# Kernel optimization log

Measured on AMD Instinct MI355X. Metric: run time of the kernel, lower is better.

The kernel has to match this reference:

```python
import jax, jax.numpy as jnp
import numpy as np

B, O, D = 64, 36, 512
G1, G2 = 512, 512  # interactor sizes
F1, F2 = 512, 512  # aggregator sizes
BN_EPS = 1e-5


def setup_inputs() -> dict:
    key = jax.random.key(0)
    ks = jax.random.split(key, 10)
    sc = 0.02
    return {
        "objs": jax.random.normal(ks[0], (B, O, D), jnp.float32),
        "W1": jax.random.normal(ks[1], (G1, 2 * D), jnp.float32) * sc,
        "b1": jax.random.normal(ks[2], (G1,), jnp.float32) * sc,
        "W2": jax.random.normal(ks[3], (G2, G1), jnp.float32) * sc,
        "b2": jax.random.normal(ks[4], (G2,), jnp.float32) * sc,
        "gamma": jnp.ones((G2,), jnp.float32),
        "beta": jnp.zeros((G2,), jnp.float32),
        "W3": jax.random.normal(ks[5], (F1, G2), jnp.float32) * sc,
        "b3": jax.random.normal(ks[6], (F1,), jnp.float32) * sc,
        "W4": jax.random.normal(ks[7], (F2, F1), jnp.float32) * sc,
        "b4": jax.random.normal(ks[8], (F2,), jnp.float32) * sc,
    }


def reference(objs, W1, b1, W2, b2, gamma, beta, W3, b3, W4, b4):
    b, o, d = objs.shape
    # make_pairs: x_full[b,k,m] = concat(v[b,m], v[b,k]) -> (b, o*o, 2d)
    v_i = jnp.broadcast_to(objs[:, None, :, :], (b, o, o, d))  # varies over m
    v_j = jnp.broadcast_to(objs[:, :, None, :], (b, o, o, d))  # varies over k
    pairs = jnp.concatenate([v_i, v_j], axis=-1).reshape(b, o * o, 2 * d)
    # interaction MLP g
    h = jax.nn.relu(jnp.einsum('bpc,gc->bpg', pairs, W1) + b1)
    x_pairs = jax.nn.relu(jnp.einsum('bpg,hg->bph', h, W2) + b2)
    # sum over pairs, BatchNorm1d (training mode: batch stats, biased var)
    s = x_pairs.sum(axis=1)  # (b, G2)
    mean = s.mean(axis=0)
    var = ((s - mean) ** 2).mean(axis=0)
    sn = (s - mean) / jnp.sqrt(var + BN_EPS) * gamma + beta
    # aggregation MLP f
    a = jax.nn.relu(sn @ W3.T + b3)
    agg = jax.nn.relu(a @ W4.T + b4)
    return agg, x_pairs
```

## Files before the change

kernel.cpp:

```cpp
#include <hip/hip_runtime.h>
#include <cstdint>
#include <cstddef>

#define B_  64
#define O_  36
#define D_  512
#define P_  (O_*O_)
#define BO_ (B_*O_)

typedef short s8v __attribute__((ext_vector_type(8)));
typedef float f4v __attribute__((ext_vector_type(4)));

__device__ __forceinline__ void bsplit(float x, short& hi, short& lo) {
    unsigned u = __float_as_uint(x);
    unsigned r = (u + 0x7FFFu + ((u >> 16) & 1u)) >> 16;
    hi = (short)r;
    float hf = __uint_as_float(r << 16);
    float d = x - hf;
    unsigned u2 = __float_as_uint(d);
    unsigned r2 = (u2 + 0x7FFFu + ((u2 >> 16) & 1u)) >> 16;
    lo = (short)r2;
}

__global__ __launch_bounds__(256) void wsplit_all(
    const float* __restrict__ W2, const float* __restrict__ W1,
    short* __restrict__ W2h, short* __restrict__ W2l,
    short* __restrict__ W1h, short* __restrict__ W1l)
{
    int i = (blockIdx.x * 256 + threadIdx.x) * 4;
    float4 w;
    short* hip_; short* lop_; int o;
    if (i < 512 * 512) {
        w = *(const float4*)&W2[i];
        hip_ = W2h; lop_ = W2l; o = i;
    } else {
        o = i - 512 * 512;
        const int n = o >> 9, d = o & 511;
        w = *(const float4*)&W1[(size_t)(n & 511) * 1024 + ((n >> 9) << 9) + d];
        hip_ = W1h; lop_ = W1l;
    }
    short h0, l0, h1, l1, h2, l2, h3, l3;
    bsplit(w.x, h0, l0); bsplit(w.y, h1, l1);
    bsplit(w.z, h2, l2); bsplit(w.w, h3, l3);
    *(short4*)&hip_[o] = make_short4(h0, h1, h2, h3);
    *(short4*)&lop_[o] = make_short4(l0, l1, l2, l3);
}

__global__ __launch_bounds__(256, 2) void uv_mfma(
    const float* __restrict__ objs,
    const short* __restrict__ W1h, const short* __restrict__ W1l,
    float* __restrict__ U, float* __restrict__ V)
{
    __shared__ short Ah[128 * 40];
    __shared__ short Al[128 * 40];
    __shared__ short Bh[128 * 40];
    __shared__ short Bl[128 * 40];

    const int tid  = threadIdx.x;
    const int lane = tid & 63;
    const int wid  = tid >> 6;
    const int wr   = wid >> 1, wc = wid & 1;
    const int rowbase = blockIdx.y * 128;
    const int colbase = blockIdx.x * 128;

    const int srow = tid >> 1;
    const int skq  = (tid & 1) * 8;
    const float* Xrow  = objs + (size_t)(rowbase + srow) * 512;
    const short* Whrow = W1h + (size_t)(colbase + srow) * 512;
    const short* Wlrow = W1l + (size_t)(colbase + srow) * 512;

    const int fr = lane & 15;
    const int sl = (lane >> 4) * 8;
    const int abase = (wr * 64 + fr) * 40 + sl;
    const int bbase = (wc * 64 + fr) * 40 + sl;

    f4v acc[4][4];
    const f4v zero = {0.f, 0.f, 0.f, 0.f};
    #pragma unroll
    for (int i = 0; i < 4; ++i)
        #pragma unroll
        for (int j = 0; j < 4; ++j) acc[i][j] = zero;

    for (int kt = 0; kt < 512; kt += 32) {
        __syncthreads();
        #pragma unroll
        for (int pass = 0; pass < 2; ++pass) {
            const int kq = skq + pass * 16;
            const float4 x0 = *(const float4*)&Xrow[kt + kq];
            const float4 x1 = *(const float4*)&Xrow[kt + kq + 4];
            float hx[8] = {x0.x, x0.y, x0.z, x0.w, x1.x, x1.y, x1.z, x1.w};
            s8v hi8, lo8;
            #pragma unroll
            for (int j = 0; j < 8; ++j) { short h, l; bsplit(hx[j], h, l); hi8[j] = h; lo8[j] = l; }
            *(s8v*)&Ah[srow * 40 + kq] = hi8;
            *(s8v*)&Al[srow * 40 + kq] = lo8;
            *(s8v*)&Bh[srow * 40 + kq] = *(const s8v*)&Whrow[kt + kq];
            *(s8v*)&Bl[srow * 40 + kq] = *(const s8v*)&Wlrow[kt + kq];
        }
        __syncthreads();

        s8v ah[4], al[4], bh[4], bl[4];
        #pragma unroll
        for (int f = 0; f < 4; ++f) {
            ah[f] = *(const s8v*)&Ah[abase + f * 640];
            al[f] = *(const s8v*)&Al[abase + f * 640];
            bh[f] = *(const s8v*)&Bh[bbase + f * 640];
            bl[f] = *(const s8v*)&Bl[bbase + f * 640];
        }
        #pragma unroll
        for (int fm = 0; fm < 4; ++fm)
            #pragma unroll
            for (int fn = 0; fn < 4; ++fn)
                acc[fm][fn] = __builtin_amdgcn_mfma_f32_16x16x32_bf16(ah[fm], bh[fn], acc[fm][fn], 0, 0, 0);
        #pragma unroll
        for (int fm = 0; fm < 4; ++fm)
            #pragma unroll
            for (int fn = 0; fn < 4; ++fn)
                acc[fm][fn] = __builtin_amdgcn_mfma_f32_16x16x32_bf16(ah[fm], bl[fn], acc[fm][fn], 0, 0, 0);
        #pragma unroll
        for (int fm = 0; fm < 4; ++fm)
            #pragma unroll
            for (int fn = 0; fn < 4; ++fn)
                acc[fm][fn] = __builtin_amdgcn_mfma_f32_16x16x32_bf16(al[fm], bh[fn], acc[fm][fn], 0, 0, 0);
    }

    float* dst = (colbase < 512) ? U : V;
    const int cb = colbase & 511;
    const int r4 = (lane >> 4) * 4;
    #pragma unroll
    for (int fm = 0; fm < 4; ++fm) {
        #pragma unroll
        for (int r = 0; r < 4; ++r) {
            const int row = rowbase + wr * 64 + fm * 16 + r4 + r;
            float* drow = &dst[(size_t)row * 512 + cb + wc * 64 + fr];
            #pragma unroll
            for (int fn = 0; fn < 4; ++fn) drow[fn * 16] = acc[fm][fn][r];
        }
    }
}

__global__ __launch_bounds__(512, 2) void pair_gemm(
    const float* __restrict__ U, const float* __restrict__ V,
    const float* __restrict__ b1,
    const short* __restrict__ W2h, const short* __restrict__ W2l,
    const float* __restrict__ b2,
    float* __restrict__ xout, float* __restrict__ s)
{
    __shared__ short Ah[128 * 40];
    __shared__ short Al[128 * 40];
    __shared__ short Bh[512 * 40];
    __shared__ short Bl[512 * 40];
    __shared__ float b1s[512];

    const int tid  = threadIdx.x;
    const int lane = tid & 63;
    const int wid  = tid >> 6;
    const int wr   = wid >> 2;
    const int wc   = wid & 3;
    const int b     = blockIdx.y;
    const int pbase = blockIdx.x * 128;

    b1s[tid] = b1[tid];

    const int arow = tid & 127;
    const int akq  = (tid >> 7) << 3;
    const int p    = pbase + arow;
    const bool valid = (p < P_);
    int ki = 0, mi = 0;
    if (valid) { ki = p / O_; mi = p - ki * O_; }
    const float* Urow = U + (size_t)(b * O_ + mi) * 512 + akq;
    const float* Vrow = V + (size_t)(b * O_ + ki) * 512 + akq;

    const short* Whrow = W2h + (size_t)tid * 512;
    const short* Wlrow = W2l + (size_t)tid * 512;

    const int fr = lane & 15;
    const int sl = (lane >> 4) << 3;
    const int abase = (wr * 64 + fr) * 40 + sl;
    const int bbase = (wc * 128 + fr) * 40 + sl;

    f4v acc[4][8];
    const f4v zero = {0.f, 0.f, 0.f, 0.f};
    #pragma unroll
    for (int i = 0; i < 4; ++i)
        #pragma unroll
        for (int j = 0; j < 8; ++j) acc[i][j] = zero;

    for (int kt = 0; kt < 512; kt += 32) {
        __syncthreads();
        {
            s8v hi8, lo8;
            if (valid) {
                const float4 u0 = *(const float4*)&Urow[kt];
                const float4 u1 = *(const float4*)&Urow[kt + 4];
                const float4 v0 = *(const float4*)&Vrow[kt];
                const float4 v1 = *(const float4*)&Vrow[kt + 4];
                const float4 c0 = *(const float4*)&b1s[kt + akq];
                const float4 c1 = *(const float4*)&b1s[kt + akq + 4];
                float hx[8];
                hx[0] = fmaxf(u0.x + v0.x + c0.x, 0.f);
                hx[1] = fmaxf(u0.y + v0.y + c0.y, 0.f);
                hx[2] = fmaxf(u0.z + v0.z + c0.z, 0.f);
                hx[3] = fmaxf(u0.w + v0.w + c0.w, 0.f);
                hx[4] = fmaxf(u1.x + v1.x + c1.x, 0.f);
                hx[5] = fmaxf(u1.y + v1.y + c1.y, 0.f);
                hx[6] = fmaxf(u1.z + v1.z + c1.z, 0.f);
                hx[7] = fmaxf(u1.w + v1.w + c1.w, 0.f);
                #pragma unroll
                for (int j = 0; j < 8; ++j) { short h, l; bsplit(hx[j], h, l); hi8[j] = h; lo8[j] = l; }
            } else {
                #pragma unroll
                for (int j = 0; j < 8; ++j) { hi8[j] = 0; lo8[j] = 0; }
            }
            *(s8v*)&Ah[arow * 40 + akq] = hi8;
            *(s8v*)&Al[arow * 40 + akq] = lo8;
        }
        #pragma unroll
        for (int c = 0; c < 4; ++c) {
            *(s8v*)&Bh[tid * 40 + c * 8] = *(const s8v*)&Whrow[kt + c * 8];
            *(s8v*)&Bl[tid * 40 + c * 8] = *(const s8v*)&Wlrow[kt + c * 8];
        }
        __syncthreads();

        s8v ah[4], al[4];
        #pragma unroll
        for (int f = 0; f < 4; ++f) {
            ah[f] = *(const s8v*)&Ah[abase + f * 640];
            al[f] = *(const s8v*)&Al[abase + f * 640];
        }
        #pragma unroll
        for (int fn = 0; fn < 8; ++fn) {
            const s8v bh = *(const s8v*)&Bh[bbase + fn * 640];
            const s8v bl = *(const s8v*)&Bl[bbase + fn * 640];
            #pragma unroll
            for (int fm = 0; fm < 4; ++fm)
                acc[fm][fn] = __builtin_amdgcn_mfma_f32_16x16x32_bf16(ah[fm], bh, acc[fm][fn], 0, 0, 0);
            #pragma unroll
            for (int fm = 0; fm < 4; ++fm)
                acc[fm][fn] = __builtin_amdgcn_mfma_f32_16x16x32_bf16(ah[fm], bl, acc[fm][fn], 0, 0, 0);
            #pragma unroll
            for (int fm = 0; fm < 4; ++fm)
                acc[fm][fn] = __builtin_amdgcn_mfma_f32_16x16x32_bf16(al[fm], bh, acc[fm][fn], 0, 0, 0);
        }
    }

    float b2v[8];
    #pragma unroll
    for (int fn = 0; fn < 8; ++fn) b2v[fn] = b2[wc * 128 + fn * 16 + fr];
    const int r4 = (lane >> 4) << 2;
    float csum[8] = {0.f, 0.f, 0.f, 0.f, 0.f, 0.f, 0.f, 0.f};
    #pragma unroll
    for (int fm = 0; fm < 4; ++fm) {
        const int prow0 = pbase + wr * 64 + fm * 16 + r4;
        #pragma unroll
        for (int r = 0; r < 4; ++r) {
            const int pp = prow0 + r;
            if (pp < P_) {
                float* xrow = &xout[(size_t)(b * P_ + pp) * 512 + wc * 128 + fr];
                #pragma unroll
                for (int fn = 0; fn < 8; ++fn) {
                    float x = fmaxf(acc[fm][fn][r] + b2v[fn], 0.f);
                    xrow[fn * 16] = x;
                    csum[fn] += x;
                }
            }
        }
    }
    #pragma unroll
    for (int fn = 0; fn < 8; ++fn) {
        csum[fn] += __shfl_xor(csum[fn], 16);
        csum[fn] += __shfl_xor(csum[fn], 32);
    }
    if (lane < 16) {
        #pragma unroll
        for (int fn = 0; fn < 8; ++fn)
            atomicAdd(&s[b * 512 + wc * 128 + fn * 16 + lane], csum[fn]);
    }
}

__global__ __launch_bounds__(512) void bn_kernel(
    const float* __restrict__ s, const float* __restrict__ gamma,
    const float* __restrict__ beta, float* __restrict__ sn)
{
    const int g = threadIdx.x;
    float mean = 0.f;
    for (int b = 0; b < B_; ++b) mean += s[b * 512 + g];
    mean *= (1.f / B_);
    float var = 0.f;
    for (int b = 0; b < B_; ++b) { const float d = s[b * 512 + g] - mean; var = fmaf(d, d, var); }
    var *= (1.f / B_);
    const float inv = 1.f / sqrtf(var + 1e-5f);
    const float ga = gamma[g], be = beta[g];
    for (int b = 0; b < B_; ++b)
        sn[b * 512 + g] = (s[b * 512 + g] - mean) * inv * ga + be;
}

__global__ __launch_bounds__(256) void mlp512(
    const float* __restrict__ x, const float* __restrict__ W,
    const float* __restrict__ bias, float* __restrict__ out)
{
    __shared__ float xs[512];
    const int b = blockIdx.y;
    const int f = blockIdx.x * 256 + threadIdx.x;
    for (int g = threadIdx.x; g < 512; g += 256) xs[g] = x[b * 512 + g];
    __syncthreads();
    float sum = 0.f;
    #pragma unroll 8
    for (int k = 0; k < 512; k += 4) {
        const float4 w4 = *(const float4*)&W[(size_t)f * 512 + k];
        const float4 x4 = *(const float4*)&xs[k];
        sum = fmaf(w4.x, x4.x, sum); sum = fmaf(w4.y, x4.y, sum);
        sum = fmaf(w4.z, x4.z, sum); sum = fmaf(w4.w, x4.w, sum);
    }
    out[b * 512 + f] = fmaxf(sum + bias[f], 0.f);
}

extern "C" void kernel_launch(void* const* d_in, const int* in_sizes, int n_in,
                              void* d_out, int out_size, void* d_ws, size_t ws_size,
                              hipStream_t stream)
{
    const float* objs  = (const float*)d_in[0];
    const float* W1    = (const float*)d_in[1];
    const float* b1    = (const float*)d_in[2];
    const float* W2    = (const float*)d_in[3];
    const float* b2    = (const float*)d_in[4];
    const float* gamma = (const float*)d_in[5];
    const float* beta  = (const float*)d_in[6];
    const float* W3    = (const float*)d_in[7];
    const float* b3    = (const float*)d_in[8];
    const float* W4    = (const float*)d_in[9];
    const float* b4    = (const float*)d_in[10];

    float* out  = (float*)d_out;
    float* xout = out + B_ * 512;

    float* U  = (float*)d_ws;
    float* V  = U  + (size_t)BO_ * 512;
    float* s  = V  + (size_t)BO_ * 512;
    float* sn = s  + B_ * 512;
    float* a  = sn + B_ * 512;
    short* W2h = (short*)(a + B_ * 512);
    short* W2l = W2h + (size_t)512 * 512;
    short* W1h = W2l + (size_t)512 * 512;
    short* W1l = W1h + (size_t)1024 * 512;

    wsplit_all<<<768, 256, 0, stream>>>(W2, W1, W2h, W2l, W1h, W1l);
    uv_mfma<<<dim3(8, 18), 256, 0, stream>>>(objs, W1h, W1l, U, V);
    hipMemsetAsync(s, 0, B_ * 512 * sizeof(float), stream);
    pair_gemm<<<dim3(11, 64), 512, 0, stream>>>(U, V, b1, W2h, W2l, b2, xout, s);
    bn_kernel<<<1, 512, 0, stream>>>(s, gamma, beta, sn);
    mlp512<<<dim3(2, B_), 256, 0, stream>>>(sn, W3, b3, a);
    mlp512<<<dim3(2, B_), 256, 0, stream>>>(a, W4, b4, out);
}
```

Before: 469.4 us.

## Retile pair GEMM to 128x128 output tiles with octet-major LDS layout

The pair GEMM block now covers 128 pairs by 128 output columns with 256 threads, instead of 128 pairs by 512 columns with 512 threads. The grid grows fourfold, adding a column dimension, and LDS is reorganized into an octet-major [k-octet][row][8] layout to avoid bank conflicts without padding. The aim is better occupancy and load balance through smaller register and LDS footprints per block. In exchange, each block now recomputes the fused U+V+b1 ReLU and bf16 split of its A tile, so that work is repeated four times across the column blocks.

Result: faster. 451.3 us (-3.9%).

```diff
diff --git a/kernel.cpp b/kernel.cpp
--- a/kernel.cpp
+++ b/kernel.cpp
@@ -139,64 +139,73 @@
     }
 }
 
-__global__ __launch_bounds__(512, 2) void pair_gemm(
+__global__ __launch_bounds__(256, 3) void pair_gemm(
     const float* __restrict__ U, const float* __restrict__ V,
     const float* __restrict__ b1,
     const short* __restrict__ W2h, const short* __restrict__ W2l,
     const float* __restrict__ b2,
     float* __restrict__ xout, float* __restrict__ s)
 {
-    __shared__ short Ah[128 * 40];
-    __shared__ short Al[128 * 40];
-    __shared__ short Bh[512 * 40];
-    __shared__ short Bl[512 * 40];
+    __shared__ short Ah[4][128][8];
+    __shared__ short Al[4][128][8];
+    __shared__ short Bh[4][128][8];
+    __shared__ short Bl[4][128][8];
     __shared__ float b1s[512];
 
     const int tid  = threadIdx.x;
     const int lane = tid & 63;
     const int wid  = tid >> 6;
-    const int wr   = wid >> 2;
-    const int wc   = wid & 3;
-    const int b     = blockIdx.y;
-    const int pbase = blockIdx.x * 128;
-
-    b1s[tid] = b1[tid];
+    const int wr   = wid >> 1, wc = wid & 1;
+    const int b       = blockIdx.z;
+    const int pbase   = blockIdx.y * 128;
+    const int colbase = blockIdx.x * 128;
+
+    for (int g = tid; g < 512; g += 256) b1s[g] = b1[g];
 
     const int arow = tid & 127;
-    const int akq  = (tid >> 7) << 3;
+    const int a0   = (tid >> 7) * 2;
     const int p    = pbase + arow;
     const bool valid = (p < P_);
     int ki = 0, mi = 0;
     if (valid) { ki = p / O_; mi = p - ki * O_; }
-    const float* Urow = U + (size_t)(b * O_ + mi) * 512 + akq;
-    const float* Vrow = V + (size_t)(b * O_ + ki) * 512 + akq;
-
-    const short* Whrow = W2h + (size_t)tid * 512;
-    const short* Wlrow = W2l + (size_t)tid * 512;
+    const float* Urow = U + (size_t)(b * O_ + mi) * 512;
+    const float* Vrow = V + (size_t)(b * O_ + ki) * 512;
+
+    const int boct = wid;
+    const int brow = lane;
+    const short* Wh0 = W2h + (size_t)(colbase + brow) * 512 + boct * 8;
+    const short* Wh1 = Wh0 + (size_t)64 * 512;
+    const short* Wl0 = W2l + (size_t)(colbase + brow) * 512 + boct * 8;
+    const short* Wl1 = Wl0 + (size_t)64 * 512;
 
     const int fr = lane & 15;
-    const int sl = (lane >> 4) << 3;
-    const int abase = (wr * 64 + fr) * 40 + sl;
-    const int bbase = (wc * 128 + fr) * 40 + sl;
-
-    f4v acc[4][8];
+    const int q  = lane >> 4;
+
+    f4v acc[4][4];
     const f4v zero = {0.f, 0.f, 0.f, 0.f};
     #pragma unroll
     for (int i = 0; i < 4; ++i)
         #pragma unroll
-        for (int j = 0; j < 8; ++j) acc[i][j] = zero;
+        for (int j = 0; j < 4; ++j) acc[i][j] = zero;
 
     for (int kt = 0; kt < 512; kt += 32) {
         __syncthreads();
-        {
+        const s8v wh0 = *(const s8v*)&Wh0[kt];
+        const s8v wh1 = *(const s8v*)&Wh1[kt];
+        const s8v wl0 = *(const s8v*)&Wl0[kt];
+        const s8v wl1 = *(const s8v*)&Wl1[kt];
+        #pragma unroll
+        for (int j = 0; j < 2; ++j) {
+            const int oct = a0 + j;
+            const int k0  = kt + oct * 8;
             s8v hi8, lo8;
             if (valid) {
-                const float4 u0 = *(const float4*)&Urow[kt];
-                const float4 u1 = *(const float4*)&Urow[kt + 4];
-                const float4 v0 = *(const float4*)&Vrow[kt];
-                const float4 v1 = *(const float4*)&Vrow[kt + 4];
-                const float4 c0 = *(const float4*)&b1s[kt + akq];
-                const float4 c1 = *(const float4*)&b1s[kt + akq + 4];
+                const float4 u0 = *(const float4*)&Urow[k0];
+                const float4 u1 = *(const float4*)&Urow[k0 + 4];
+                const float4 v0 = *(const float4*)&Vrow[k0];
+                const float4 v1 = *(const float4*)&Vrow[k0 + 4];
+                const float4 c0 = *(const float4*)&b1s[k0];
+                const float4 c1 = *(const float4*)&b1s[k0 + 4];
                 float hx[8];
                 hx[0] = fmaxf(u0.x + v0.x + c0.x, 0.f);
                 hx[1] = fmaxf(u0.y + v0.y + c0.y, 0.f);
@@ -207,48 +216,50 @@
                 hx[6] = fmaxf(u1.z + v1.z + c1.z, 0.f);
                 hx[7] = fmaxf(u1.w + v1.w + c1.w, 0.f);
                 #pragma unroll
-                for (int j = 0; j < 8; ++j) { short h, l; bsplit(hx[j], h, l); hi8[j] = h; lo8[j] = l; }
+                for (int e = 0; e < 8; ++e) { short h, l; bsplit(hx[e], h, l); hi8[e] = h; lo8[e] = l; }
             } else {
                 #pragma unroll
-                for (int j = 0; j < 8; ++j) { hi8[j] = 0; lo8[j] = 0; }
+                for (int e = 0; e < 8; ++e) { hi8[e] = 0; lo8[e] = 0; }
             }
-            *(s8v*)&Ah[arow * 40 + akq] = hi8;
-            *(s8v*)&Al[arow * 40 + akq] = lo8;
-        }
-        #pragma unroll
-        for (int c = 0; c < 4; ++c) {
-            *(s8v*)&Bh[tid * 40 + c * 8] = *(const s8v*)&Whrow[kt + c * 8];
-            *(s8v*)&Bl[tid * 40 + c * 8] = *(const s8v*)&Wlrow[kt + c * 8];
-        }
+            *(s8v*)&Ah[oct][arow][0] = hi8;
+            *(s8v*)&Al[oct][arow][0] = lo8;
+        }
+        *(s8v*)&Bh[boct][brow][0]      = wh0;
+        *(s8v*)&Bh[boct][64 + brow][0] = wh1;
+        *(s8v*)&Bl[boct][brow][0]      = wl0;
+        *(s8v*)&Bl[boct][64 + brow][0] = wl1;
         __syncthreads();
 
-        s8v ah[4], al[4];
+        s8v ah[4], al[4], bh[4], bl[4];
         #pragma unroll
         for (int f = 0; f < 4; ++f) {
-            ah[f] = *(const s8v*)&Ah[abase + f * 640];
-            al[f] = *(const s8v*)&Al[abase + f * 640];
-        }
-        #pragma unroll
-        for (int fn = 0; fn < 8; ++fn) {
-            const s8v bh = *(const s8v*)&Bh[bbase + fn * 640];
-            const s8v bl = *(const s8v*)&Bl[bbase + fn * 640];
-            #pragma unroll
-            for (int fm = 0; fm < 4; ++fm)
-                acc[fm][fn] = __builtin_amdgcn_mfma_f32_16x16x32_bf16(ah[fm], bh, acc[fm][fn], 0, 0, 0);
-            #pragma unroll
-            for (int fm = 0; fm < 4; ++fm)
-                acc[fm][fn] = __builtin_amdgcn_mfma_f32_16x16x32_bf16(ah[fm], bl, acc[fm][fn], 0, 0, 0);
-            #pragma unroll
-            for (int fm = 0; fm < 4; ++fm)
-                acc[fm][fn] = __builtin_amdgcn_mfma_f32_16x16x32_bf16(al[fm], bh, acc[fm][fn], 0, 0, 0);
-        }
-    }
-
-    float b2v[8];
-    #pragma unroll
-    for (int fn = 0; fn < 8; ++fn) b2v[fn] = b2[wc * 128 + fn * 16 + fr];
-    const int r4 = (lane >> 4) << 2;
-    float csum[8] = {0.f, 0.f, 0.f, 0.f, 0.f, 0.f, 0.f, 0.f};
+            ah[f] = *(const s8v*)&Ah[q][wr * 64 + f * 16 + fr][0];
+            al[f] = *(const s8v*)&Al[q][wr * 64 + f * 16 + fr][0];
+            bh[f] = *(const s8v*)&Bh[q][wc * 64 + f * 16 + fr][0];
+            bl[f] = *(const s8v*)&Bl[q][wc * 64 + f * 16 + fr][0];
+        }
+        #pragma unroll
+        for (int fm = 0; fm < 4; ++fm)
+            #pragma unroll
+            for (int fn = 0; fn < 4; ++fn)
+                acc[fm][fn] = __builtin_amdgcn_mfma_f32_16x16x32_bf16(ah[fm], bh[fn], acc[fm][fn], 0, 0, 0);
+        #pragma unroll
+        for (int fm = 0; fm < 4; ++fm)
+            #pragma unroll
+            for (int fn = 0; fn < 4; ++fn)
+                acc[fm][fn] = __builtin_amdgcn_mfma_f32_16x16x32_bf16(ah[fm], bl[fn], acc[fm][fn], 0, 0, 0);
+        #pragma unroll
+        for (int fm = 0; fm < 4; ++fm)
+            #pragma unroll
+            for (int fn = 0; fn < 4; ++fn)
+                acc[fm][fn] = __builtin_amdgcn_mfma_f32_16x16x32_bf16(al[fm], bh[fn], acc[fm][fn], 0, 0, 0);
+    }
+
+    float b2v[4];
+    #pragma unroll
+    for (int fn = 0; fn < 4; ++fn) b2v[fn] = b2[colbase + wc * 64 + fn * 16 + fr];
+    const int r4 = (lane >> 4) * 4;
+    float csum[4] = {0.f, 0.f, 0.f, 0.f};
     #pragma unroll
     for (int fm = 0; fm < 4; ++fm) {
         const int prow0 = pbase + wr * 64 + fm * 16 + r4;
@@ -256,9 +267,9 @@
         for (int r = 0; r < 4; ++r) {
             const int pp = prow0 + r;
             if (pp < P_) {
-                float* xrow = &xout[(size_t)(b * P_ + pp) * 512 + wc * 128 + fr];
+                float* xrow = &xout[(size_t)(b * P_ + pp) * 512 + colbase + wc * 64 + fr];
                 #pragma unroll
-                for (int fn = 0; fn < 8; ++fn) {
+                for (int fn = 0; fn < 4; ++fn) {
                     float x = fmaxf(acc[fm][fn][r] + b2v[fn], 0.f);
                     xrow[fn * 16] = x;
                     csum[fn] += x;
@@ -267,14 +278,14 @@
         }
     }
     #pragma unroll
-    for (int fn = 0; fn < 8; ++fn) {
+    for (int fn = 0; fn < 4; ++fn) {
         csum[fn] += __shfl_xor(csum[fn], 16);
         csum[fn] += __shfl_xor(csum[fn], 32);
     }
     if (lane < 16) {
         #pragma unroll
-        for (int fn = 0; fn < 8; ++fn)
-            atomicAdd(&s[b * 512 + wc * 128 + fn * 16 + lane], csum[fn]);
+        for (int fn = 0; fn < 4; ++fn)
+            atomicAdd(&s[b * 512 + colbase + wc * 64 + fn * 16 + lane], csum[fn]);
     }
 }
 
@@ -347,7 +358,7 @@
     wsplit_all<<<768, 256, 0, stream>>>(W2, W1, W2h, W2l, W1h, W1l);
     uv_mfma<<<dim3(8, 18), 256, 0, stream>>>(objs, W1h, W1l, U, V);
     hipMemsetAsync(s, 0, B_ * 512 * sizeof(float), stream);
-    pair_gemm<<<dim3(11, 64), 512, 0, stream>>>(U, V, b1, W2h, W2l, b2, xout, s);
+    pair_gemm<<<dim3(4, 11, B_), 256, 0, stream>>>(U, V, b1, W2h, W2l, b2, xout, s);
     bn_kernel<<<1, 512, 0, stream>>>(s, gamma, beta, sn);
     mlp512<<<dim3(2, B_), 256, 0, stream>>>(sn, W3, b3, a);
     mlp512<<<dim3(2, B_), 256, 0, stream>>>(a, W4, b4, out);
```
